# Optimization experiments

Hardware: AMD Instinct MI355X
Metric: run time of the kernel (lower is better)

The kernel has to match this reference:

```python
import jax, jax.numpy as jnp
import numpy as np

N = 50000        # nodes
E = 800000       # edges (avg degree 16)
F = 64           # node_feature
H = 128          # dim_h
C = 10           # num_classes
G = 512          # graphs in batch
BN_EPS = 1e-5


def setup_inputs() -> dict:
    key = jax.random.key(0)
    ks = iter(jax.random.split(key, 40))
    inp = {}
    inp['x'] = jax.random.normal(next(ks), (N, F), dtype=jnp.float32)
    inp['edge_index'] = jax.random.randint(next(ks), (2, E), 0, N, dtype=jnp.int32)
    inp['batch'] = jnp.sort(jax.random.randint(next(ks), (N,), 0, G, dtype=jnp.int32))
    # GINConv MLP params (Linear, BatchNorm1d(eval), ReLU, Linear, ReLU) x3
    in_dims = [F, H, H]
    for i in range(1, 4):
        d_in = in_dims[i - 1]
        inp[f'c{i}_w1'] = jax.random.normal(next(ks), (d_in, H), dtype=jnp.float32) * 0.05
        inp[f'c{i}_b1'] = jnp.zeros((H,), dtype=jnp.float32)
        inp[f'c{i}_g'] = jnp.ones((H,), dtype=jnp.float32)
        inp[f'c{i}_be'] = jnp.zeros((H,), dtype=jnp.float32)
        inp[f'c{i}_m'] = jax.random.normal(next(ks), (H,), dtype=jnp.float32) * 0.01
        inp[f'c{i}_v'] = jax.random.uniform(next(ks), (H,), dtype=jnp.float32) + 0.5
        inp[f'c{i}_w2'] = jax.random.normal(next(ks), (H, H), dtype=jnp.float32) * 0.05
        inp[f'c{i}_b2'] = jnp.zeros((H,), dtype=jnp.float32)
    inp['lin1_w'] = jax.random.normal(next(ks), (3 * H, 3 * H), dtype=jnp.float32) * 0.05
    inp['lin1_b'] = jnp.zeros((3 * H,), dtype=jnp.float32)
    inp['lin2_w'] = jax.random.normal(next(ks), (3 * H, C), dtype=jnp.float32) * 0.05
    inp['lin2_b'] = jnp.zeros((C,), dtype=jnp.float32)
    return inp


def _mlp(h, w1, b1, g, be, m, v, w2, b2):
    h = h @ w1 + b1
    h = (h - m) * jax.lax.rsqrt(v + BN_EPS) * g + be  # BatchNorm1d (eval)
    h = jax.nn.relu(h)
    return jax.nn.relu(h @ w2 + b2)


def _gin_conv(x, src, dst, w1, b1, g, be, m, v, w2, b2):
    # GINConv, eps=0: MLP(x_i + sum_{j->i} x_j)
    agg = jax.ops.segment_sum(x[src], dst, num_segments=N)
    return _mlp(x + agg, w1, b1, g, be, m, v, w2, b2)


def reference(x, edge_index, batch,
              c1_w1, c1_b1, c1_g, c1_be, c1_m, c1_v, c1_w2, c1_b2,
              c2_w1, c2_b1, c2_g, c2_be, c2_m, c2_v, c2_w2, c2_b2,
              c3_w1, c3_b1, c3_g, c3_be, c3_m, c3_v, c3_w2, c3_b2,
              lin1_w, lin1_b, lin2_w, lin2_b):
    src, dst = edge_index[0], edge_index[1]
    h1 = _gin_conv(x, src, dst, c1_w1, c1_b1, c1_g, c1_be, c1_m, c1_v, c1_w2, c1_b2)
    h2 = _gin_conv(h1, src, dst, c2_w1, c2_b1, c2_g, c2_be, c2_m, c2_v, c2_w2, c2_b2)
    h3 = _gin_conv(h2, src, dst, c3_w1, c3_b1, c3_g, c3_be, c3_m, c3_v, c3_w2, c3_b2)
    p1 = jax.ops.segment_sum(h1, batch, num_segments=G)  # global_add_pool
    p2 = jax.ops.segment_sum(h2, batch, num_segments=G)
    p3 = jax.ops.segment_sum(h3, batch, num_segments=G)
    h = jnp.concatenate((p1, p2, p3), axis=1)  # [G, 3H]
    h = jax.nn.relu(h @ lin1_w + lin1_b)
    # dropout is identity in eval mode
    h = h @ lin2_w + lin2_b
    return jax.nn.log_softmax(h, axis=1)
```

## Files before the change

kernel.cpp:

```cpp
#include <hip/hip_runtime.h>
#include <math.h>
#include <stdint.h>

static constexpr int NN = 50000;
static constexpr int NE = 800000;
static constexpr int NG = 512;
static constexpr int NB = (NN + 255) / 256;
static constexpr float BNEPS = 1e-5f;

typedef __bf16 bf16x8 __attribute__((ext_vector_type(8)));
typedef __bf16 bf16x2 __attribute__((ext_vector_type(2)));
typedef float f32x4 __attribute__((ext_vector_type(4)));

__device__ __forceinline__ uint32_t pack_bf16(float x, float y) {
    bf16x2 v; v[0] = (__bf16)x; v[1] = (__bf16)y;
    return __builtin_bit_cast(uint32_t, v);
}
__device__ __forceinline__ float2 unpack_bf16(uint32_t u) {
    bf16x2 v = __builtin_bit_cast(bf16x2, u);
    return make_float2((float)v[0], (float)v[1]);
}


__global__ void degree_kernel(const int* __restrict__ dst, int* __restrict__ deg,
                              uint16_t* __restrict__ rank) {
    int e = blockIdx.x * blockDim.x + threadIdx.x;
    if (e < NE) rank[e] = (uint16_t)atomicAdd(&deg[dst[e]], 1);
}

__global__ __launch_bounds__(256) void blocksum_kernel(const int* __restrict__ deg,
                                                       int* __restrict__ bsum) {
    int i = blockIdx.x * 256 + threadIdx.x;
    int v = (i < NN) ? deg[i] : 0;
#pragma unroll
    for (int off = 32; off; off >>= 1) v += __shfl_down(v, off, 64);
    __shared__ int s[4];
    if ((threadIdx.x & 63) == 0) s[threadIdx.x >> 6] = v;
    __syncthreads();
    if (threadIdx.x == 0) bsum[blockIdx.x] = s[0] + s[1] + s[2] + s[3];
}

__global__ __launch_bounds__(256) void scanb_kernel(const int* __restrict__ bsum,
                                                    int* __restrict__ bscan,
                                                    int* __restrict__ row_ptr) {
    __shared__ int s[256];
    int t = threadIdx.x;
    int v = (t < NB) ? bsum[t] : 0;
    s[t] = v;
    __syncthreads();
    for (int off = 1; off < 256; off <<= 1) {
        int u = (t >= off) ? s[t - off] : 0;
        __syncthreads();
        s[t] += u;
        __syncthreads();
    }
    if (t < NB) bscan[t] = s[t] - v;
    if (t == NB - 1) row_ptr[NN] = s[t];
}

__global__ __launch_bounds__(256) void scanfinal_kernel(const int* __restrict__ deg,
                                                        const int* __restrict__ bscan,
                                                        int* __restrict__ row_ptr) {
    __shared__ int s[256];
    int t = threadIdx.x;
    int i = blockIdx.x * 256 + t;
    int v = (i < NN) ? deg[i] : 0;
    s[t] = v;
    __syncthreads();
    for (int off = 1; off < 256; off <<= 1) {
        int u = (t >= off) ? s[t - off] : 0;
        __syncthreads();
        s[t] += u;
        __syncthreads();
    }
    if (i < NN) row_ptr[i] = bscan[blockIdx.x] + s[t] - v;
}

__global__ void fill_kernel(const int* __restrict__ src, const int* __restrict__ dst,
                            const int* __restrict__ row_ptr, const uint16_t* __restrict__ rank,
                            uint16_t* __restrict__ cols) {
    int e = blockIdx.x * blockDim.x + threadIdx.x;
    if (e < NE) cols[row_ptr[dst[e]] + (int)rank[e]] = (uint16_t)src[e];
}


__global__ void prep_kernel(const float* __restrict__ x, __bf16* __restrict__ xb,
                            const float* s0, const float* s1, const float* s2,
                            const float* s3, const float* s4, const float* s5,
                            const float* s6,
                            __bf16* d0, __bf16* d1, __bf16* d2,
                            __bf16* d3, __bf16* d4, __bf16* d5, __bf16* d6) {
    int i = blockIdx.x * blockDim.x + threadIdx.x;
    if (i < 800000) {
        float4 v = *(const float4*)&x[i * 4];
        xb[i * 4 + 0] = (__bf16)v.x;
        xb[i * 4 + 1] = (__bf16)v.y;
        xb[i * 4 + 2] = (__bf16)v.z;
        xb[i * 4 + 3] = (__bf16)v.w;
        return;
    }
    int j = i - 800000;
    if (j < 8192) {
        int l = j;           int n = l / 64,  k = l % 64;  d0[l] = (__bf16)s0[k * 128 + n];
    } else if (j < 24576) {
        int l = j - 8192;    int n = l / 128, k = l % 128; d1[l] = (__bf16)s1[k * 128 + n];
    } else if (j < 40960) {
        int l = j - 24576;   int n = l / 128, k = l % 128; d2[l] = (__bf16)s2[k * 128 + n];
    } else if (j < 57344) {
        int l = j - 40960;   int n = l / 128, k = l % 128; d3[l] = (__bf16)s3[k * 128 + n];
    } else if (j < 73728) {
        int l = j - 57344;   int n = l / 128, k = l % 128; d4[l] = (__bf16)s4[k * 128 + n];
    } else if (j < 90112) {
        int l = j - 73728;   int n = l / 128, k = l % 128; d5[l] = (__bf16)s5[k * 128 + n];
    } else if (j < 237568) {
        int l = j - 90112;   int n = l / 384, k = l % 384; d6[l] = (__bf16)s6[k * 384 + n];
    }
}


template <int DWPR>
__global__ __launch_bounds__(512) void gather_pass_kernel(const __bf16* __restrict__ in,
                                                          const int* __restrict__ row_ptr,
                                                          const uint16_t* __restrict__ cols,
                                                          __bf16* __restrict__ agg) {
    int wid = threadIdx.x >> 6;
    int sub = (threadIdx.x & 63) >> 4;
    int l16 = threadIdx.x & 15;
    int node = (blockIdx.x * 8 + wid) * 4 + sub;
    if (node >= NN) return;
    int off = blockIdx.y * 16 + l16;
    const uint32_t* inu = (const uint32_t*)in;
    uint32_t* aggu = (uint32_t*)agg;
    int beg = row_ptr[node], end = row_ptr[node + 1];
    float2 a0 = unpack_bf16(inu[(size_t)node * DWPR + off]);
    float2 a1 = make_float2(0.f, 0.f);
    int i = beg;
    for (; i + 4 <= end; i += 4) {
        int c0 = cols[i], c1 = cols[i + 1], c2 = cols[i + 2], c3 = cols[i + 3];
        uint32_t u0 = inu[(size_t)c0 * DWPR + off];
        uint32_t u1 = inu[(size_t)c1 * DWPR + off];
        uint32_t u2 = inu[(size_t)c2 * DWPR + off];
        uint32_t u3 = inu[(size_t)c3 * DWPR + off];
        float2 v0 = unpack_bf16(u0), v1 = unpack_bf16(u1);
        float2 v2 = unpack_bf16(u2), v3 = unpack_bf16(u3);
        a0.x += v0.x + v1.x; a0.y += v0.y + v1.y;
        a1.x += v2.x + v3.x; a1.y += v2.y + v3.y;
    }
    for (; i < end; ++i) {
        float2 v = unpack_bf16(inu[(size_t)cols[i] * DWPR + off]);
        a0.x += v.x; a0.y += v.y;
    }
    aggu[(size_t)node * DWPR + off] = pack_bf16(a0.x + a1.x, a0.y + a1.y);
}


template <int K, bool WOUT>
__global__ __launch_bounds__(512, 1) void mlp_mfma_kernel(
    const __bf16* __restrict__ agg,
    const __bf16* __restrict__ w1t,
    const float* __restrict__ b1,
    const float* __restrict__ g, const float* __restrict__ be,
    const float* __restrict__ m, const float* __restrict__ v,
    const __bf16* __restrict__ w2t,
    const float* __restrict__ b2,
    __bf16* __restrict__ out,
    const int* __restrict__ batch,
    float* __restrict__ p,
    int col_off)
{
    constexpr int KP = K + 8;
    constexpr int KP2 = 136;
    __shared__ alignas(16) __bf16 sA[64 * KP];
    __shared__ alignas(16) __bf16 sW1[128 * KP];
    __shared__ alignas(16) __bf16 sW2[128 * KP2];
    __shared__ alignas(16) __bf16 sT[64 * KP2];
    __shared__ alignas(16) __bf16 sOut[64 * KP2];
    __shared__ int sBatch[64];

    int tid = threadIdx.x;
    int wid = tid >> 6, lane = tid & 63;
    int wr = wid >> 1, wc = wid & 1;
    int l15 = lane & 15, lq = lane >> 4;
    int rowbase = blockIdx.x * 64;

    for (int idx = tid; idx < 64 * (K / 8); idx += 512) {
        int r = idx / (K / 8), kc = idx % (K / 8);
        int n = rowbase + r;
        uint4 val = make_uint4(0, 0, 0, 0);
        if (n < NN) val = *(const uint4*)&agg[(size_t)n * K + kc * 8];
        *(uint4*)&sA[r * KP + kc * 8] = val;
    }
    for (int idx = tid; idx < 128 * (K / 8); idx += 512) {
        int n = idx / (K / 8), kc = idx % (K / 8);
        *(uint4*)&sW1[n * KP + kc * 8] = *(const uint4*)&w1t[n * K + kc * 8];
    }
    for (int idx = tid; idx < 128 * 16; idx += 512) {
        int n = idx >> 4, kc = idx & 15;
        *(uint4*)&sW2[n * KP2 + kc * 8] = *(const uint4*)&w2t[n * 128 + kc * 8];
    }
    if (tid < 64) {
        int n = rowbase + tid;
        sBatch[tid] = (n < NN) ? batch[n] : -1;
    }
    __syncthreads();

    f32x4 acc[4] = {};
#pragma unroll
    for (int ks = 0; ks < K / 32; ++ks) {
        bf16x8 a = *(const bf16x8*)&sA[(wr * 16 + l15) * KP + ks * 32 + lq * 8];
#pragma unroll
        for (int nf = 0; nf < 4; ++nf) {
            bf16x8 b = *(const bf16x8*)&sW1[(wc * 64 + nf * 16 + l15) * KP + ks * 32 + lq * 8];
            acc[nf] = __builtin_amdgcn_mfma_f32_16x16x32_bf16(a, b, acc[nf], 0, 0, 0);
        }
    }
#pragma unroll
    for (int nf = 0; nf < 4; ++nf) {
        int c = wc * 64 + nf * 16 + l15;
        float sc = g[c] * rsqrtf(v[c] + BNEPS);
        float sh = be[c] + (b1[c] - m[c]) * sc;
#pragma unroll
        for (int r = 0; r < 4; ++r) {
            int row = wr * 16 + lq * 4 + r;
            float t = fmaxf(acc[nf][r] * sc + sh, 0.f);
            sT[row * KP2 + c] = (__bf16)t;
        }
    }
    __syncthreads();

    f32x4 acc2[4] = {};
#pragma unroll
    for (int ks = 0; ks < 4; ++ks) {
        bf16x8 a = *(const bf16x8*)&sT[(wr * 16 + l15) * KP2 + ks * 32 + lq * 8];
#pragma unroll
        for (int nf = 0; nf < 4; ++nf) {
            bf16x8 b = *(const bf16x8*)&sW2[(wc * 64 + nf * 16 + l15) * KP2 + ks * 32 + lq * 8];
            acc2[nf] = __builtin_amdgcn_mfma_f32_16x16x32_bf16(a, b, acc2[nf], 0, 0, 0);
        }
    }
#pragma unroll
    for (int nf = 0; nf < 4; ++nf) {
        int c = wc * 64 + nf * 16 + l15;
        float bb = b2[c];
#pragma unroll
        for (int r = 0; r < 4; ++r) {
            int row = wr * 16 + lq * 4 + r;
            float o = fmaxf(acc2[nf][r] + bb, 0.f);
            sOut[row * KP2 + c] = (__bf16)o;
        }
    }
    __syncthreads();

    if constexpr (WOUT) {
        for (int idx = tid; idx < 64 * 16; idx += 512) {
            int r = idx >> 4, kc = idx & 15;
            int n = rowbase + r;
            if (n < NN)
                *(uint4*)&out[(size_t)n * 128 + kc * 8] = *(const uint4*)&sOut[r * KP2 + kc * 8];
        }
    }

    {
        int f = tid & 127;
        int chunk = tid >> 7;
        float pacc = 0.f;
        int cur = -1;
#pragma unroll
        for (int i = 0; i < 16; ++i) {
            int row = chunk * 16 + i;
            int b = sBatch[row];
            if (b < 0) break;
            if (b != cur) {
                if (cur >= 0) atomicAdd(&p[cur * 384 + col_off + f], pacc);
                pacc = 0.f;
                cur = b;
            }
            pacc += (float)sOut[row * KP2 + f];
        }
        if (cur >= 0) atomicAdd(&p[cur * 384 + col_off + f], pacc);
    }
}


__global__ __launch_bounds__(512, 1) void head1_kernel(const float* __restrict__ p,
                                                       const __bf16* __restrict__ lin1t,
                                                       const float* __restrict__ b1,
                                                       float* __restrict__ hrelu) {
    constexpr int KPA = 392;
    constexpr int KPW = 136;
    __shared__ alignas(16) __bf16 sA[64 * KPA];
    __shared__ alignas(16) __bf16 sW[128 * KPW];

    int tid = threadIdx.x;
    int wid = tid >> 6, lane = tid & 63;
    int wr = wid >> 1, wc = wid & 1;
    int l15 = lane & 15, lq = lane >> 4;
    int rowbase = blockIdx.x * 64;
    int colbase = blockIdx.y * 128;

    for (int idx = tid; idx < 64 * 48; idx += 512) {
        int r = idx / 48, kc = idx % 48;
        const float* srcp = &p[(rowbase + r) * 384 + kc * 8];
        float4 v0 = *(const float4*)srcp;
        float4 v1 = *(const float4*)(srcp + 4);
        bf16x8 o;
        o[0] = (__bf16)v0.x; o[1] = (__bf16)v0.y; o[2] = (__bf16)v0.z; o[3] = (__bf16)v0.w;
        o[4] = (__bf16)v1.x; o[5] = (__bf16)v1.y; o[6] = (__bf16)v1.z; o[7] = (__bf16)v1.w;
        *(bf16x8*)&sA[r * KPA + kc * 8] = o;
    }

    f32x4 acc[4] = {};
#pragma unroll
    for (int kchunk = 0; kchunk < 3; ++kchunk) {
        for (int idx = tid; idx < 128 * 16; idx += 512) {
            int n = idx >> 4, kc = idx & 15;
            *(uint4*)&sW[n * KPW + kc * 8] =
                *(const uint4*)&lin1t[(colbase + n) * 384 + kchunk * 128 + kc * 8];
        }
        __syncthreads();
#pragma unroll
        for (int ks = 0; ks < 4; ++ks) {
            bf16x8 a = *(const bf16x8*)&sA[(wr * 16 + l15) * KPA + kchunk * 128 + ks * 32 + lq * 8];
#pragma unroll
            for (int nf = 0; nf < 4; ++nf) {
                bf16x8 b = *(const bf16x8*)&sW[(wc * 64 + nf * 16 + l15) * KPW + ks * 32 + lq * 8];
                acc[nf] = __builtin_amdgcn_mfma_f32_16x16x32_bf16(a, b, acc[nf], 0, 0, 0);
            }
        }
        __syncthreads();
    }
#pragma unroll
    for (int nf = 0; nf < 4; ++nf) {
        int col = colbase + wc * 64 + nf * 16 + l15;
        float bb = b1[col];
#pragma unroll
        for (int r = 0; r < 4; ++r) {
            int row = rowbase + wr * 16 + lq * 4 + r;
            hrelu[row * 384 + col] = fmaxf(acc[nf][r] + bb, 0.f);
        }
    }
}


__global__ __launch_bounds__(256) void head2_kernel(const float* __restrict__ hrelu,
                                                    const float* __restrict__ w2,
                                                    const float* __restrict__ b2,
                                                    float* __restrict__ out) {
    int wid = threadIdx.x >> 6, lane = threadIdx.x & 63;
    int gidx = blockIdx.x * 4 + wid;
    const float* hr = &hrelu[gidx * 384 + lane * 6];
    float h[6];
#pragma unroll
    for (int u = 0; u < 6; ++u) h[u] = hr[u];
    float logit[10];
#pragma unroll
    for (int c = 0; c < 10; ++c) {
        float s = 0.f;
#pragma unroll
        for (int u = 0; u < 6; ++u) s = fmaf(h[u], w2[(lane * 6 + u) * 10 + c], s);
#pragma unroll
        for (int off = 32; off; off >>= 1) s += __shfl_xor(s, off, 64);
        logit[c] = s + b2[c];
    }
    float mx = logit[0];
#pragma unroll
    for (int c = 1; c < 10; ++c) mx = fmaxf(mx, logit[c]);
    float se = 0.f;
#pragma unroll
    for (int c = 0; c < 10; ++c) se += expf(logit[c] - mx);
    float lse = logf(se);
    float val = 0.f;
#pragma unroll
    for (int c = 0; c < 10; ++c) if (lane == c) val = logit[c];
    if (lane < 10) out[gidx * 10 + lane] = val - mx - lse;
}


static inline char* align_up(char* ptr, size_t a) {
    return (char*)(((uintptr_t)ptr + a - 1) & ~(uintptr_t)(a - 1));
}

extern "C" void kernel_launch(void* const* d_in, const int* in_sizes, int n_in,
                              void* d_out, int out_size, void* d_ws, size_t ws_size,
                              hipStream_t stream) {
    const float* x = (const float*)d_in[0];
    const int* ei = (const int*)d_in[1];
    const int* batch = (const int*)d_in[2];
    const float* c_w1[3], *c_b1[3], *c_g[3], *c_be[3], *c_m[3], *c_v[3], *c_w2[3], *c_b2[3];
    for (int i = 0; i < 3; ++i) {
        int base = 3 + i * 8;
        c_w1[i] = (const float*)d_in[base + 0];
        c_b1[i] = (const float*)d_in[base + 1];
        c_g[i]  = (const float*)d_in[base + 2];
        c_be[i] = (const float*)d_in[base + 3];
        c_m[i]  = (const float*)d_in[base + 4];
        c_v[i]  = (const float*)d_in[base + 5];
        c_w2[i] = (const float*)d_in[base + 6];
        c_b2[i] = (const float*)d_in[base + 7];
    }
    const float* lin1_w = (const float*)d_in[27];
    const float* lin1_b = (const float*)d_in[28];
    const float* lin2_w = (const float*)d_in[29];
    const float* lin2_b = (const float*)d_in[30];
    const int* src = ei;
    const int* dst = ei + NE;
    float* out = (float*)d_out;

    char* ws = (char*)d_ws;
    __bf16* xb  = (__bf16*)ws; ws = align_up(ws + (size_t)NN * 64 * 2, 256);
    __bf16* agg = (__bf16*)ws; ws = align_up(ws + (size_t)NN * 128 * 2, 256);
    __bf16* hA  = (__bf16*)ws; ws = align_up(ws + (size_t)NN * 128 * 2, 256);
    __bf16* hB  = (__bf16*)ws; ws = align_up(ws + (size_t)NN * 128 * 2, 256);
    float* p    = (float*)ws;  ws = align_up(ws + (size_t)NG * 384 * 4, 256);
    float* hrelu = (float*)ws; ws = align_up(ws + (size_t)NG * 384 * 4, 256);
    int* csr_row = (int*)ws;   ws = align_up(ws + (size_t)(NN + 1) * 4, 256);
    int* cursor  = (int*)ws;   ws = align_up(ws + (size_t)NN * 4, 256);
    uint16_t* csr_src = (uint16_t*)ws; ws = align_up(ws + (size_t)NE * 2, 256);
    uint16_t* rank    = (uint16_t*)ws; ws = align_up(ws + (size_t)NE * 2, 256);
    int* bsum    = (int*)ws;   ws = align_up(ws + (size_t)NB * 4, 256);
    int* bscan   = (int*)ws;   ws = align_up(ws + (size_t)NB * 4, 256);
    __bf16* w1t[3]; __bf16* w2t[3];
    for (int i = 0; i < 3; ++i) {
        int K = (i == 0) ? 64 : 128;
        w1t[i] = (__bf16*)ws; ws = align_up(ws + (size_t)128 * K * 2, 256);
        w2t[i] = (__bf16*)ws; ws = align_up(ws + (size_t)128 * 128 * 2, 256);
    }
    __bf16* lin1t = (__bf16*)ws; ws = align_up(ws + (size_t)384 * 384 * 2, 256);

    hipMemsetAsync(cursor, 0, (size_t)NN * 4, stream);
    degree_kernel<<<(NE + 255) / 256, 256, 0, stream>>>(dst, cursor, rank);
    blocksum_kernel<<<NB, 256, 0, stream>>>(cursor, bsum);
    scanb_kernel<<<1, 256, 0, stream>>>(bsum, bscan, csr_row);
    scanfinal_kernel<<<NB, 256, 0, stream>>>(cursor, bscan, csr_row);
    fill_kernel<<<(NE + 255) / 256, 256, 0, stream>>>(src, dst, csr_row, rank, csr_src);
    hipMemsetAsync(p, 0, (size_t)NG * 384 * 4, stream);

    prep_kernel<<<(800000 + 237568 + 255) / 256, 256, 0, stream>>>(
        x, xb,
        c_w1[0], c_w1[1], c_w1[2], c_w2[0], c_w2[1], c_w2[2], lin1_w,
        w1t[0], w1t[1], w1t[2], w2t[0], w2t[1], w2t[2], lin1t);

    const int GATHER_X = (NN + 31) / 32;
    const int MLP_BLOCKS = (NN + 63) / 64;

    gather_pass_kernel<32><<<dim3(GATHER_X, 2), 512, 0, stream>>>(xb, csr_row, csr_src, agg);
    mlp_mfma_kernel<64, true><<<MLP_BLOCKS, 512, 0, stream>>>(agg, w1t[0], c_b1[0], c_g[0], c_be[0],
                                                              c_m[0], c_v[0], w2t[0], c_b2[0], hA,
                                                              batch, p, 0);

    gather_pass_kernel<64><<<dim3(GATHER_X, 4), 512, 0, stream>>>(hA, csr_row, csr_src, agg);
    mlp_mfma_kernel<128, true><<<MLP_BLOCKS, 512, 0, stream>>>(agg, w1t[1], c_b1[1], c_g[1], c_be[1],
                                                               c_m[1], c_v[1], w2t[1], c_b2[1], hB,
                                                               batch, p, 128);

    gather_pass_kernel<64><<<dim3(GATHER_X, 4), 512, 0, stream>>>(hB, csr_row, csr_src, agg);
    mlp_mfma_kernel<128, false><<<MLP_BLOCKS, 512, 0, stream>>>(agg, w1t[2], c_b1[2], c_g[2], c_be[2],
                                                                c_m[2], c_v[2], w2t[2], c_b2[2], nullptr,
                                                                batch, p, 256);

    head1_kernel<<<dim3(8, 3), 512, 0, stream>>>(p, lin1t, lin1_b, hrelu);
    head2_kernel<<<128, 256, 0, stream>>>(hrelu, lin2_w, lin2_b, out);
}
```

Baseline: 288.1 us.

## Slice gather by feature with edge-parallel lanes; shrink MLP LDS for occupancy

The gather kernel is rewritten so each block handles one feature slice, blockIdx.x & 7 selecting it. Within a wave, lanes split across edges (64/DWS edge groups) and are combined with xor-shuffle reductions. This replaces one node per 16 lanes walking the edges serially, and aims to raise memory-level parallelism and cache locality per feature slice. The MLP kernel reuses one LDS buffer for W1 then W2, and one for input and output, raising launch bounds to 4 blocks/SM. The cost is an extra W2 load phase after a barrier and shuffle-reduction overhead per node.

Result: slower. 499.7 us (+73.4%).

```diff
diff --git a/kernel.cpp b/kernel.cpp
--- a/kernel.cpp
+++ b/kernel.cpp
@@ -118,44 +118,45 @@
 }
 
 
-template <int DWPR>
-__global__ __launch_bounds__(512) void gather_pass_kernel(const __bf16* __restrict__ in,
-                                                          const int* __restrict__ row_ptr,
-                                                          const uint16_t* __restrict__ cols,
-                                                          __bf16* __restrict__ agg) {
-    int wid = threadIdx.x >> 6;
-    int sub = (threadIdx.x & 63) >> 4;
-    int l16 = threadIdx.x & 15;
-    int node = (blockIdx.x * 8 + wid) * 4 + sub;
-    if (node >= NN) return;
-    int off = blockIdx.y * 16 + l16;
+template <int DWPR, int DWS>
+__global__ __launch_bounds__(512) void gather_slice_kernel(const __bf16* __restrict__ in,
+                                                           const int* __restrict__ row_ptr,
+                                                           const uint16_t* __restrict__ cols,
+                                                           __bf16* __restrict__ agg) {
+    constexpr int NEG = 64 / DWS;
+    int slice = blockIdx.x & 7;
+    int wid = threadIdx.x >> 6, lane = threadIdx.x & 63;
+    int nodebase = (blockIdx.x >> 3) * 32 + wid * 4;
+    int eg = lane / DWS, d = lane % DWS;
+    int off = slice * DWS + d;
     const uint32_t* inu = (const uint32_t*)in;
     uint32_t* aggu = (uint32_t*)agg;
-    int beg = row_ptr[node], end = row_ptr[node + 1];
-    float2 a0 = unpack_bf16(inu[(size_t)node * DWPR + off]);
-    float2 a1 = make_float2(0.f, 0.f);
-    int i = beg;
-    for (; i + 4 <= end; i += 4) {
-        int c0 = cols[i], c1 = cols[i + 1], c2 = cols[i + 2], c3 = cols[i + 3];
-        uint32_t u0 = inu[(size_t)c0 * DWPR + off];
-        uint32_t u1 = inu[(size_t)c1 * DWPR + off];
-        uint32_t u2 = inu[(size_t)c2 * DWPR + off];
-        uint32_t u3 = inu[(size_t)c3 * DWPR + off];
-        float2 v0 = unpack_bf16(u0), v1 = unpack_bf16(u1);
-        float2 v2 = unpack_bf16(u2), v3 = unpack_bf16(u3);
-        a0.x += v0.x + v1.x; a0.y += v0.y + v1.y;
-        a1.x += v2.x + v3.x; a1.y += v2.y + v3.y;
-    }
-    for (; i < end; ++i) {
-        float2 v = unpack_bf16(inu[(size_t)cols[i] * DWPR + off]);
-        a0.x += v.x; a0.y += v.y;
-    }
-    aggu[(size_t)node * DWPR + off] = pack_bf16(a0.x + a1.x, a0.y + a1.y);
+
+#pragma unroll
+    for (int t = 0; t < 4; ++t) {
+        int node = nodebase + t;
+        if (node >= NN) break;
+        int beg = row_ptr[node], end = row_ptr[node + 1];
+        float2 a = make_float2(0.f, 0.f);
+        for (int i = beg + eg; i < end; i += NEG) {
+            float2 v = unpack_bf16(inu[(size_t)(int)cols[i] * DWPR + off]);
+            a.x += v.x; a.y += v.y;
+        }
+#pragma unroll
+        for (int o = DWS; o < 64; o <<= 1) {
+            a.x += __shfl_xor(a.x, o, 64);
+            a.y += __shfl_xor(a.y, o, 64);
+        }
+        if (lane < DWS) {
+            float2 s = unpack_bf16(inu[(size_t)node * DWPR + off]);
+            aggu[(size_t)node * DWPR + off] = pack_bf16(a.x + s.x, a.y + s.y);
+        }
+    }
 }
 
 
 template <int K, bool WOUT>
-__global__ __launch_bounds__(512, 1) void mlp_mfma_kernel(
+__global__ __launch_bounds__(512, 4) void mlp_mfma_kernel(
     const __bf16* __restrict__ agg,
     const __bf16* __restrict__ w1t,
     const float* __restrict__ b1,
@@ -170,11 +171,9 @@
 {
     constexpr int KP = K + 8;
     constexpr int KP2 = 136;
-    __shared__ alignas(16) __bf16 sA[64 * KP];
-    __shared__ alignas(16) __bf16 sW1[128 * KP];
-    __shared__ alignas(16) __bf16 sW2[128 * KP2];
+    __shared__ alignas(16) __bf16 sAO[64 * KP2];
+    __shared__ alignas(16) __bf16 sW[128 * KP2];
     __shared__ alignas(16) __bf16 sT[64 * KP2];
-    __shared__ alignas(16) __bf16 sOut[64 * KP2];
     __shared__ int sBatch[64];
 
     int tid = threadIdx.x;
@@ -188,15 +187,11 @@
         int n = rowbase + r;
         uint4 val = make_uint4(0, 0, 0, 0);
         if (n < NN) val = *(const uint4*)&agg[(size_t)n * K + kc * 8];
-        *(uint4*)&sA[r * KP + kc * 8] = val;
+        *(uint4*)&sAO[r * KP + kc * 8] = val;
     }
     for (int idx = tid; idx < 128 * (K / 8); idx += 512) {
         int n = idx / (K / 8), kc = idx % (K / 8);
-        *(uint4*)&sW1[n * KP + kc * 8] = *(const uint4*)&w1t[n * K + kc * 8];
-    }
-    for (int idx = tid; idx < 128 * 16; idx += 512) {
-        int n = idx >> 4, kc = idx & 15;
-        *(uint4*)&sW2[n * KP2 + kc * 8] = *(const uint4*)&w2t[n * 128 + kc * 8];
+        *(uint4*)&sW[n * KP + kc * 8] = *(const uint4*)&w1t[n * K + kc * 8];
     }
     if (tid < 64) {
         int n = rowbase + tid;
@@ -207,10 +202,10 @@
     f32x4 acc[4] = {};
 #pragma unroll
     for (int ks = 0; ks < K / 32; ++ks) {
-        bf16x8 a = *(const bf16x8*)&sA[(wr * 16 + l15) * KP + ks * 32 + lq * 8];
+        bf16x8 a = *(const bf16x8*)&sAO[(wr * 16 + l15) * KP + ks * 32 + lq * 8];
 #pragma unroll
         for (int nf = 0; nf < 4; ++nf) {
-            bf16x8 b = *(const bf16x8*)&sW1[(wc * 64 + nf * 16 + l15) * KP + ks * 32 + lq * 8];
+            bf16x8 b = *(const bf16x8*)&sW[(wc * 64 + nf * 16 + l15) * KP + ks * 32 + lq * 8];
             acc[nf] = __builtin_amdgcn_mfma_f32_16x16x32_bf16(a, b, acc[nf], 0, 0, 0);
         }
     }
@@ -228,13 +223,19 @@
     }
     __syncthreads();
 
+    for (int idx = tid; idx < 128 * 16; idx += 512) {
+        int n = idx >> 4, kc = idx & 15;
+        *(uint4*)&sW[n * KP2 + kc * 8] = *(const uint4*)&w2t[n * 128 + kc * 8];
+    }
+    __syncthreads();
+
     f32x4 acc2[4] = {};
 #pragma unroll
     for (int ks = 0; ks < 4; ++ks) {
         bf16x8 a = *(const bf16x8*)&sT[(wr * 16 + l15) * KP2 + ks * 32 + lq * 8];
 #pragma unroll
         for (int nf = 0; nf < 4; ++nf) {
-            bf16x8 b = *(const bf16x8*)&sW2[(wc * 64 + nf * 16 + l15) * KP2 + ks * 32 + lq * 8];
+            bf16x8 b = *(const bf16x8*)&sW[(wc * 64 + nf * 16 + l15) * KP2 + ks * 32 + lq * 8];
             acc2[nf] = __builtin_amdgcn_mfma_f32_16x16x32_bf16(a, b, acc2[nf], 0, 0, 0);
         }
     }
@@ -246,7 +247,7 @@
         for (int r = 0; r < 4; ++r) {
             int row = wr * 16 + lq * 4 + r;
             float o = fmaxf(acc2[nf][r] + bb, 0.f);
-            sOut[row * KP2 + c] = (__bf16)o;
+            sAO[row * KP2 + c] = (__bf16)o;
         }
     }
     __syncthreads();
@@ -256,7 +257,7 @@
             int r = idx >> 4, kc = idx & 15;
             int n = rowbase + r;
             if (n < NN)
-                *(uint4*)&out[(size_t)n * 128 + kc * 8] = *(const uint4*)&sOut[r * KP2 + kc * 8];
+                *(uint4*)&out[(size_t)n * 128 + kc * 8] = *(const uint4*)&sAO[r * KP2 + kc * 8];
         }
     }
 
@@ -275,7 +276,7 @@
                 pacc = 0.f;
                 cur = b;
             }
-            pacc += (float)sOut[row * KP2 + f];
+            pacc += (float)sAO[row * KP2 + f];
         }
         if (cur >= 0) atomicAdd(&p[cur * 384 + col_off + f], pacc);
     }
@@ -440,20 +441,20 @@
         c_w1[0], c_w1[1], c_w1[2], c_w2[0], c_w2[1], c_w2[2], lin1_w,
         w1t[0], w1t[1], w1t[2], w2t[0], w2t[1], w2t[2], lin1t);
 
-    const int GATHER_X = (NN + 31) / 32;
+    const int GATHER_BLOCKS = 8 * ((NN + 31) / 32);
     const int MLP_BLOCKS = (NN + 63) / 64;
 
-    gather_pass_kernel<32><<<dim3(GATHER_X, 2), 512, 0, stream>>>(xb, csr_row, csr_src, agg);
+    gather_slice_kernel<32, 4><<<GATHER_BLOCKS, 512, 0, stream>>>(xb, csr_row, csr_src, agg);
     mlp_mfma_kernel<64, true><<<MLP_BLOCKS, 512, 0, stream>>>(agg, w1t[0], c_b1[0], c_g[0], c_be[0],
                                                               c_m[0], c_v[0], w2t[0], c_b2[0], hA,
                                                               batch, p, 0);
 
-    gather_pass_kernel<64><<<dim3(GATHER_X, 4), 512, 0, stream>>>(hA, csr_row, csr_src, agg);
+    gather_slice_kernel<64, 8><<<GATHER_BLOCKS, 512, 0, stream>>>(hA, csr_row, csr_src, agg);
     mlp_mfma_kernel<128, true><<<MLP_BLOCKS, 512, 0, stream>>>(agg, w1t[1], c_b1[1], c_g[1], c_be[1],
                                                                c_m[1], c_v[1], w2t[1], c_b2[1], hB,
                                                                batch, p, 128);
 
-    gather_pass_kernel<64><<<dim3(GATHER_X, 4), 512, 0, stream>>>(hB, csr_row, csr_src, agg);
+    gather_slice_kernel<64, 8><<<GATHER_BLOCKS, 512, 0, stream>>>(hB, csr_row, csr_src, agg);
     mlp_mfma_kernel<128, false><<<MLP_BLOCKS, 512, 0, stream>>>(agg, w1t[2], c_b1[2], c_g[2], c_be[2],
                                                                 c_m[2], c_v[2], w2t[2], c_b2[2], nullptr,
                                                                 batch, p, 256);
```
